# Kernel optimization log

Hardware: AMD Instinct MI355X
Metric: run time of the kernel (lower is better)

The kernel has to match this reference:

```python
import jax, jax.numpy as jnp
import numpy as np

B, T, D_IN, H, C = 16, 8192, 4, 256, 11


def setup_inputs() -> dict:
    key = jax.random.key(0)
    ks = jax.random.split(key, 9)
    sequence = jax.random.normal(ks[0], (B, T, D_IN), jnp.float32)
    # lengths in [7*T/8, T] so every sequence has mask[:,0]=True (torchcrf requirement)
    lengths = (T - jax.random.randint(ks[1], (B,), 0, T // 8)).astype(jnp.int64)
    labels = jax.random.randint(ks[2], (B, T), 0, C).astype(jnp.int64)
    W_enc = jax.random.normal(ks[3], (D_IN, H), jnp.float32) / np.float32(np.sqrt(D_IN))
    b_enc = jnp.zeros((H,), jnp.float32)
    W_emit = jax.random.normal(ks[4], (H, C), jnp.float32) / np.float32(np.sqrt(H))
    b_emit = jnp.zeros((C,), jnp.float32)
    start_trans = jax.random.normal(ks[5], (C,), jnp.float32) * 0.1
    trans = jax.random.normal(ks[6], (C, C), jnp.float32) * 0.1
    end_trans = jax.random.normal(ks[7], (C,), jnp.float32) * 0.1
    return dict(sequence=sequence, W_enc=W_enc, b_enc=b_enc, W_emit=W_emit,
                b_emit=b_emit, start_trans=start_trans, trans=trans,
                end_trans=end_trans, lengths=lengths, labels=labels)


def reference(sequence, W_enc, b_enc, W_emit, b_emit, start_trans, trans, end_trans, lengths, labels):
    # encoder (Linear + ReLU) and emission projection
    hidden = jax.nn.relu(sequence @ W_enc + b_enc)        # [B,T,H]
    em = hidden @ W_emit + b_emit                          # [B,T,C]
    mask = jnp.arange(T)[None, :] < lengths[:, None]       # [B,T] bool
    maskf = mask.astype(em.dtype)
    tags = jnp.where(labels == -100, 0, labels)            # -100 -> 0 as in compute_loss

    # ---- numerator: score of the gold path (torchcrf _compute_score) ----
    em_tag = jnp.take_along_axis(em, tags[..., None], axis=2)[..., 0]   # [B,T]
    trans_tag = trans[tags[:, :-1], tags[:, 1:]]                        # [B,T-1]
    num = start_trans[tags[:, 0]] + em_tag[:, 0]
    num = num + jnp.sum(maskf[:, 1:] * (trans_tag + em_tag[:, 1:]), axis=1)
    last_tag = tags[jnp.arange(B), lengths - 1]
    num = num + end_trans[last_tag]

    # ---- denominator: log partition via forward algorithm (torchcrf _compute_normalizer) ----
    alpha0 = start_trans[None, :] + em[:, 0]               # [B,C]
    em_rest = jnp.swapaxes(em[:, 1:], 0, 1)                # [T-1,B,C]
    mask_rest = jnp.swapaxes(mask[:, 1:], 0, 1)            # [T-1,B]

    def step(alpha, inp):
        em_t, m_t = inp
        nxt = jax.nn.logsumexp(alpha[:, :, None] + trans[None] + em_t[:, None, :], axis=1)
        return jnp.where(m_t[:, None], nxt, alpha), None

    alpha, _ = jax.lax.scan(step, alpha0, (em_rest, mask_rest))
    den = jax.nn.logsumexp(alpha + end_trans[None, :], axis=1)  # [B]

    # reduction='mean' over batch, loss = -log_likelihood
    return -jnp.mean(num - den)
```

## Files before the change

### kernel.cpp

```cpp
#include <hip/hip_runtime.h>
#include <hip/hip_bf16.h>

#define B_   16
#define T_   8192
#define H_   256
#define C_   11
#define KCH  256
#define LCH  32
#define KL   64

typedef __attribute__((ext_vector_type(8))) short short8;
typedef __attribute__((ext_vector_type(4))) float f32x4;

__global__ __launch_bounds__(256) void k_em(
    const float* __restrict__ seq, const float* __restrict__ Wenc,
    const float* __restrict__ benc, const float* __restrict__ Wemit,
    const float* __restrict__ bemit, const float* __restrict__ trans,
    const float* __restrict__ startt, const float* __restrict__ endt,
    const int* __restrict__ lengths, const int* __restrict__ labels,
    unsigned short* __restrict__ expem, float* __restrict__ numpart,
    unsigned* __restrict__ counter)
{
    __shared__ float ldsWpack[2048];
    __shared__ float ldsWemit[4096];
    __shared__ float red[4];
    int tid = threadIdx.x;
    if (blockIdx.x == 0 && tid == 0) counter[0] = 0;

    for (int idx = tid; idx < 2048; idx += 256) {
        int h = idx >> 3, s = idx & 7;
        float v = 0.f;
        if (s < 4) v = Wenc[s * H_ + h];
        else if (s == 4) v = benc[h];
        ldsWpack[idx] = v;
    }
    for (int idx = tid; idx < 4096; idx += 256) {
        int h = idx >> 4, c = idx & 15;
        ldsWemit[idx] = (c < C_) ? Wemit[h * C_ + c] : 0.f;
    }
    __syncthreads();

    int wid = tid >> 6, lane = tid & 63;
    int g = lane >> 4, li = lane & 15;
    int b0 = blockIdx.x >> 5;
    int tb0 = (blockIdx.x & 31) * 256 + wid * 64;
    size_t grow0 = (size_t)b0 * T_ + tb0;

    float4 xs[4];
#pragma unroll
    for (int tt = 0; tt < 4; tt++)
        xs[tt] = *(const float4*)(seq + (grow0 + tt * 16 + li) * 4);

    f32x4 acc[4];
#pragma unroll
    for (int tt = 0; tt < 4; tt++) acc[tt] = (f32x4){0.f, 0.f, 0.f, 0.f};

#pragma unroll 1
    for (int kb = 0; kb < 8; kb++) {
        float We[8][5], wm[8];
#pragma unroll
        for (int e = 0; e < 8; e++) {
            int h = 32 * kb + 4 * g + (e & 3) + 16 * (e >> 2);
            float4 w4 = *(const float4*)&ldsWpack[h * 8];
            We[e][0] = w4.x; We[e][1] = w4.y; We[e][2] = w4.z; We[e][3] = w4.w;
            We[e][4] = ldsWpack[h * 8 + 4];
            wm[e] = ldsWemit[h * 16 + li];
        }
        unsigned a0, a1, a2, a3;
        asm("v_cvt_pk_bf16_f32 %0, %1, %2" : "=v"(a0) : "v"(wm[0]), "v"(wm[1]));
        asm("v_cvt_pk_bf16_f32 %0, %1, %2" : "=v"(a1) : "v"(wm[2]), "v"(wm[3]));
        asm("v_cvt_pk_bf16_f32 %0, %1, %2" : "=v"(a2) : "v"(wm[4]), "v"(wm[5]));
        asm("v_cvt_pk_bf16_f32 %0, %1, %2" : "=v"(a3) : "v"(wm[6]), "v"(wm[7]));
        union { short8 s8; uint4 u4; } au;
        au.u4 = make_uint4(a0, a1, a2, a3);

#pragma unroll
        for (int tt = 0; tt < 4; tt++) {
            float4 x = xs[tt];
            float hv[8];
#pragma unroll
            for (int e = 0; e < 8; e++) {
                float h = fmaf(x.x, We[e][0],
                          fmaf(x.y, We[e][1],
                          fmaf(x.z, We[e][2],
                          fmaf(x.w, We[e][3], We[e][4]))));
                hv[e] = fmaxf(h, 0.f);
            }
            unsigned u0, u1, u2, u3;
            asm("v_cvt_pk_bf16_f32 %0, %1, %2" : "=v"(u0) : "v"(hv[0]), "v"(hv[1]));
            asm("v_cvt_pk_bf16_f32 %0, %1, %2" : "=v"(u1) : "v"(hv[2]), "v"(hv[3]));
            asm("v_cvt_pk_bf16_f32 %0, %1, %2" : "=v"(u2) : "v"(hv[4]), "v"(hv[5]));
            asm("v_cvt_pk_bf16_f32 %0, %1, %2" : "=v"(u3) : "v"(hv[6]), "v"(hv[7]));
            union { short8 s8; uint4 u4; } bfu;
            bfu.u4 = make_uint4(u0, u1, u2, u3);
            acc[tt] = __builtin_amdgcn_mfma_f32_16x16x32_bf16(au.s8, bfu.s8, acc[tt], 0, 0, 0);
        }
    }

    int len = lengths[b0];
    const int* lab = labels + (size_t)b0 * T_;
    float bm[4];
#pragma unroll
    for (int r = 0; r < 4; r++) {
        int c = 4 * g + r;
        bm[r] = (c < C_) ? bemit[c] : 0.f;
    }

    float nacc = 0.f;
#pragma unroll
    for (int tt = 0; tt < 4; tt++) {
        float em0 = acc[tt].x + bm[0];
        float em1 = acc[tt].y + bm[1];
        float em2 = acc[tt].z + bm[2];
        float em3 = acc[tt].w + bm[3];

        int t = tb0 + tt * 16 + li;
        int tg = lab[t]; tg = tg < 0 ? 0 : tg;
        if (g == (tg >> 2) && t < len) {
            int r = tg & 3;
            float emtg = r == 0 ? em0 : r == 1 ? em1 : r == 2 ? em2 : em3;
            float contrib;
            if (t == 0) {
                contrib = startt[tg] + emtg;
            } else {
                int tp = lab[t - 1]; tp = tp < 0 ? 0 : tp;
                contrib = trans[tp * C_ + tg] + emtg;
            }
            if (t == len - 1) contrib += endt[tg];
            nacc += contrib;
        }

        if (g < 3) {
            float e0 = __expf(em0), e1 = __expf(em1);
            float e2 = __expf(em2), e3 = __expf(em3);
            unsigned u0, u1;
            asm("v_cvt_pk_bf16_f32 %0, %1, %2" : "=v"(u0) : "v"(e0), "v"(e1));
            asm("v_cvt_pk_bf16_f32 %0, %1, %2" : "=v"(u1) : "v"(e2), "v"(e3));
            *(uint2*)(expem + (grow0 + tt * 16 + li) * 16 + g * 4) = make_uint2(u0, u1);
        }
    }

#pragma unroll
    for (int off = 32; off > 0; off >>= 1) nacc += __shfl_down(nacc, off);
    if (lane == 0) red[wid] = nacc;
    __syncthreads();
    if (tid == 0) numpart[blockIdx.x] = red[0] + red[1] + red[2] + red[3];
}

__device__ __forceinline__ void combineRow(const float* __restrict__ A,
                                           const float* __restrict__ Bm,
                                           float* __restrict__ D, int i)
{
    float a[C_];
#pragma unroll
    for (int kk = 0; kk < C_; kk++) a[kk] = A[i * 12 + kk];
    float als = A[i * 12 + 11];
    float m = Bm[11];
#pragma unroll
    for (int kk = 1; kk < C_; kk++) m = fmaxf(m, Bm[kk * 12 + 11]);
    float wv[C_];
#pragma unroll
    for (int kk = 0; kk < C_; kk++)
        wv[kk] = a[kk] * __expf(Bm[kk * 12 + 11] - m);
    float outv[C_];
#pragma unroll
    for (int j = 0; j < C_; j++) outv[j] = wv[0] * Bm[j];
#pragma unroll
    for (int kk = 1; kk < C_; kk++)
#pragma unroll
        for (int j = 0; j < C_; j++)
            outv[j] = fmaf(wv[kk], Bm[kk * 12 + j], outv[j]);
    float s = 0.f;
#pragma unroll
    for (int j = 0; j < C_; j++) s += outv[j];
    float rr = 1.f / s;
#pragma unroll
    for (int j = 0; j < C_; j++) D[i * 12 + j] = outv[j] * rr;
    D[i * 12 + 11] = als + m + __logf(s);
}

__global__ __launch_bounds__(256, 4) void k_chunks(
    const float* __restrict__ trans, const int* __restrict__ lengths,
    const unsigned short* __restrict__ expem, float* __restrict__ G)
{
    __shared__ float Mb[4][192];
    int tid = threadIdx.x;
    int wave = tid >> 6, lane = tid & 63;
    int i = lane & 15, g = lane >> 4;

    int bk = blockIdx.x;
    int b = bk >> 6;
    int k = ((bk & 63) << 2) | wave;
    int t0 = 1 + k * LCH;
    int len = lengths[b];
    int tl = t0 + LCH; if (len < tl) tl = len;
    int nact = tl - t0;

    const unsigned short* emp = expem + ((size_t)b * T_ + t0) * 16 + 4 * g;

    uint2 R[8][4];
#pragma unroll
    for (int q = 0; q < 16; q++)
        R[q >> 2][q & 3] = *(const uint2*)(emp + (size_t)q * 16);

    float af[4];
#pragma unroll
    for (int e = 0; e < 4; e++) {
        int kk = 4 * g + e;
        af[e] = (i < C_ && kk < C_) ? __expf(trans[kk * C_ + i]) : 0.f;
    }
    unsigned a0, a1;
    asm("v_cvt_pk_bf16_f32 %0, %1, %2" : "=v"(a0) : "v"(af[0]), "v"(af[1]));
    asm("v_cvt_pk_bf16_f32 %0, %1, %2" : "=v"(a1) : "v"(af[2]), "v"(af[3]));
    union { short8 s8; uint4 u4; } A; A.u4 = make_uint4(a0, a1, 0u, 0u);

    float p0 = (4 * g + 0 == i) ? 1.f : 0.f;
    float p1 = (4 * g + 1 == i) ? 1.f : 0.f;
    float p2 = (4 * g + 2 == i) ? 1.f : 0.f;
    float p3 = (4 * g + 3 == i) ? 1.f : 0.f;
    float ls = 0.f;

#pragma unroll
    for (int su = 0; su < 8; su++) {
        if (su < 4) {
#pragma unroll
            for (int q = 0; q < 4; q++)
                R[su + 4][q] = *(const uint2*)(emp + (size_t)((su + 4) * 4 + q) * 16);
        }
#pragma unroll
        for (int ss = 0; ss < 4; ss++) {
            if (su * 4 + ss < nact) {
                unsigned b0u, b1u;
                asm("v_cvt_pk_bf16_f32 %0, %1, %2" : "=v"(b0u) : "v"(p0), "v"(p1));
                asm("v_cvt_pk_bf16_f32 %0, %1, %2" : "=v"(b1u) : "v"(p2), "v"(p3));
                union { short8 s8; uint4 u4; } Bf; Bf.u4 = make_uint4(b0u, b1u, 0u, 0u);
                f32x4 acc = __builtin_amdgcn_mfma_f32_16x16x32_bf16(
                    A.s8, Bf.s8, (f32x4){0.f, 0.f, 0.f, 0.f}, 0, 0, 0);
                uint2 emu = R[su][ss];
                p0 = acc.x * __uint_as_float(emu.x << 16);
                p1 = acc.y * __uint_as_float(emu.x & 0xffff0000u);
                p2 = acc.z * __uint_as_float(emu.y << 16);
                p3 = acc.w * __uint_as_float(emu.y & 0xffff0000u);
            }
        }
        float part = (p0 + p1) + (p2 + p3);
        part += __shfl_xor(part, 16);
        part += __shfl_xor(part, 32);
        float r = 1.f / part;
        p0 *= r; p1 *= r; p2 *= r; p3 *= r;
        ls += __logf(part);
    }

    if (i < C_ && g < 3) {
        float w3 = (g == 2) ? ls : p3;
        *(float4*)&Mb[wave][i * 12 + 4 * g] = make_float4(p0, p1, p2, w3);
    }
    __syncthreads();

    if ((wave == 0 || wave == 2) && lane < C_)
        combineRow(Mb[wave], Mb[wave + 1], Mb[wave], lane);
    __syncthreads();

    if (wave == 0 && lane < C_) {
        float out[12];
        {
            const float* Aa = Mb[0]; const float* Bm = Mb[2];
            float a[C_];
#pragma unroll
            for (int kk = 0; kk < C_; kk++) a[kk] = Aa[lane * 12 + kk];
            float als = Aa[lane * 12 + 11];
            float m = Bm[11];
#pragma unroll
            for (int kk = 1; kk < C_; kk++) m = fmaxf(m, Bm[kk * 12 + 11]);
            float wv[C_];
#pragma unroll
            for (int kk = 0; kk < C_; kk++)
                wv[kk] = a[kk] * __expf(Bm[kk * 12 + 11] - m);
            float outv[C_];
#pragma unroll
            for (int j = 0; j < C_; j++) outv[j] = wv[0] * Bm[j];
#pragma unroll
            for (int kk = 1; kk < C_; kk++)
#pragma unroll
                for (int j = 0; j < C_; j++)
                    outv[j] = fmaf(wv[kk], Bm[kk * 12 + j], outv[j]);
            float s = 0.f;
#pragma unroll
            for (int j = 0; j < C_; j++) s += outv[j];
            float rr = 1.f / s;
#pragma unroll
            for (int j = 0; j < C_; j++) out[j] = outv[j] * rr;
            out[11] = als + m + __logf(s);
        }
        float* o = G + ((size_t)b * KL + (bk & 63)) * 132 + lane * 12;
        *(float4*)(o + 0) = make_float4(out[0], out[1], out[2], out[3]);
        *(float4*)(o + 4) = make_float4(out[4], out[5], out[6], out[7]);
        *(float4*)(o + 8) = make_float4(out[8], out[9], out[10], out[11]);
    }
}

__global__ __launch_bounds__(512, 1) void k_comb(
    const float* __restrict__ startt, const float* __restrict__ endt,
    const unsigned short* __restrict__ expem, const float* __restrict__ G0,
    const float* __restrict__ numpart, float* __restrict__ dens,
    unsigned* __restrict__ counter, float* __restrict__ out)
{
    __shared__ float M[KL * 132];
    int b = blockIdx.x, tid = threadIdx.x;

    float numb = 0.f;
    if (tid < 64) {
        float v = (tid < 32) ? numpart[b * 32 + tid] : 0.f;
#pragma unroll
        for (int off = 32; off > 0; off >>= 1) v += __shfl_down(v, off);
        numb = v;
    }

    const float4* src = (const float4*)(G0 + (size_t)b * KL * 132);
    float4* dst = (float4*)M;
#pragma unroll 4
    for (int idx = tid; idx < KL * 132 / 4; idx += 512) dst[idx] = src[idx];
    __syncthreads();

    for (int stride = 1; stride < KL; stride <<= 1) {
        int npair = KL / (2 * stride);
        for (int task = tid; task < npair * C_; task += 512) {
            int p = task / C_, i = task - p * C_;
            float* A  = M + (size_t)(2 * stride * p) * 132;
            float* Bm = M + (size_t)(2 * stride * p + stride) * 132;
            combineRow(A, Bm, A, i);
        }
        __syncthreads();
    }

    if (tid == 0) {
        const float* Cm = M;
        const unsigned short* em0 = expem + (size_t)b * T_ * 16;
        float av[C_];
        float mm = -1e30f;
#pragma unroll
        for (int i2 = 0; i2 < C_; i2++) {
            float e0 = __uint_as_float((unsigned)em0[i2] << 16);
            av[i2] = startt[i2] + __logf(e0) + Cm[i2 * 12 + 11];
            mm = fmaxf(mm, av[i2]);
        }
        float S[C_];
#pragma unroll
        for (int j = 0; j < C_; j++) S[j] = 0.f;
#pragma unroll
        for (int i2 = 0; i2 < C_; i2++) {
            float e = __expf(av[i2] - mm);
#pragma unroll
            for (int j = 0; j < C_; j++) S[j] = fmaf(e, Cm[i2 * 12 + j], S[j]);
        }
        float tot = 0.f;
#pragma unroll
        for (int j = 0; j < C_; j++) tot += S[j] * __expf(endt[j]);
        float den = __logf(tot) + mm;

        float loss = numb - den;
        __hip_atomic_store(&dens[b], loss, __ATOMIC_RELEASE, __HIP_MEMORY_SCOPE_AGENT);
        unsigned old = __hip_atomic_fetch_add(counter, 1u, __ATOMIC_ACQ_REL,
                                              __HIP_MEMORY_SCOPE_AGENT);
        if (old == B_ - 1) {
            float s = 0.f;
#pragma unroll
            for (int j = 0; j < B_; j++)
                s += __hip_atomic_load(&dens[j], __ATOMIC_ACQUIRE,
                                       __HIP_MEMORY_SCOPE_AGENT);
            out[0] = -s / (float)B_;
        }
    }
}

extern "C" void kernel_launch(void* const* d_in, const int* in_sizes, int n_in,
                              void* d_out, int out_size, void* d_ws, size_t ws_size,
                              hipStream_t stream) {
    const float* seq    = (const float*)d_in[0];
    const float* Wenc   = (const float*)d_in[1];
    const float* benc   = (const float*)d_in[2];
    const float* Wemit  = (const float*)d_in[3];
    const float* bemit  = (const float*)d_in[4];
    const float* startt = (const float*)d_in[5];
    const float* trans  = (const float*)d_in[6];
    const float* endt   = (const float*)d_in[7];
    const int*   lengths= (const int*)d_in[8];
    const int*   labels = (const int*)d_in[9];

    char* w = (char*)d_ws;
    unsigned short* expem  = (unsigned short*)w;
    float*          G0     = (float*)(w + 4194304);
    float*          numpart= (float*)(w + 4734976);
    float*          dens   = (float*)(w + 4737024);
    unsigned*       counter= (unsigned*)(w + 4737088);
    float*          out    = (float*)d_out;

    k_em<<<512, 256, 0, stream>>>(seq, Wenc, benc, Wemit, bemit, trans,
                                  startt, endt, lengths, labels,
                                  expem, numpart, counter);
    k_chunks<<<1024, 256, 0, stream>>>(trans, lengths, expem, G0);
    k_comb<<<B_, 512, 0, stream>>>(startt, endt, expem, G0, numpart,
                                   dens, counter, out);
}
```

Before: 45.23 us.

## Fuse emission and chunk-scan kernels, keeping exp-emissions in LDS

Merges the emission kernel and the chunked forward-algorithm kernel into one, so each block computes bf16 exp-emissions into shared memory and then runs the MFMA-based chunk product on 64-step chunks per wave. The global expem buffer round-trip and one kernel launch go away, and the first-timestep emissions are written to a small side buffer for the final combine. In exchange, each wave's serial chain grows from 32 to 64 steps, the fused kernel uses more LDS, and the combine tree shrinks from 64 to 32 chunks per batch.

```diff
diff --git a/kernel.cpp b/kernel.cpp
--- a/kernel.cpp
+++ b/kernel.cpp
@@ -5,25 +5,58 @@
 #define T_   8192
 #define H_   256
 #define C_   11
-#define KCH  256
-#define LCH  32
-#define KL   64
+#define KL   32
 
 typedef __attribute__((ext_vector_type(8))) short short8;
 typedef __attribute__((ext_vector_type(4))) float f32x4;
 
-__global__ __launch_bounds__(256) void k_em(
+__device__ __forceinline__ void combineRow(const float* __restrict__ A,
+                                           const float* __restrict__ Bm,
+                                           float* __restrict__ D, int i)
+{
+    float a[C_];
+#pragma unroll
+    for (int kk = 0; kk < C_; kk++) a[kk] = A[i * 12 + kk];
+    float als = A[i * 12 + 11];
+    float m = Bm[11];
+#pragma unroll
+    for (int kk = 1; kk < C_; kk++) m = fmaxf(m, Bm[kk * 12 + 11]);
+    float wv[C_];
+#pragma unroll
+    for (int kk = 0; kk < C_; kk++)
+        wv[kk] = a[kk] * __expf(Bm[kk * 12 + 11] - m);
+    float outv[C_];
+#pragma unroll
+    for (int j = 0; j < C_; j++) outv[j] = wv[0] * Bm[j];
+#pragma unroll
+    for (int kk = 1; kk < C_; kk++)
+#pragma unroll
+        for (int j = 0; j < C_; j++)
+            outv[j] = fmaf(wv[kk], Bm[kk * 12 + j], outv[j]);
+    float s = 0.f;
+#pragma unroll
+    for (int j = 0; j < C_; j++) s += outv[j];
+    float rr = 1.f / s;
+#pragma unroll
+    for (int j = 0; j < C_; j++) D[i * 12 + j] = outv[j] * rr;
+    D[i * 12 + 11] = als + m + __logf(s);
+}
+
+__global__ __launch_bounds__(256) void k_fused(
     const float* __restrict__ seq, const float* __restrict__ Wenc,
     const float* __restrict__ benc, const float* __restrict__ Wemit,
     const float* __restrict__ bemit, const float* __restrict__ trans,
     const float* __restrict__ startt, const float* __restrict__ endt,
     const int* __restrict__ lengths, const int* __restrict__ labels,
-    unsigned short* __restrict__ expem, float* __restrict__ numpart,
-    unsigned* __restrict__ counter)
+    float* __restrict__ G, float* __restrict__ numpart,
+    float* __restrict__ em0f, unsigned* __restrict__ counter)
 {
     __shared__ float ldsWpack[2048];
     __shared__ float ldsWemit[4096];
+    __shared__ unsigned emLds[256 * 8];
+    __shared__ float Mb[4][192];
     __shared__ float red[4];
+
     int tid = threadIdx.x;
     if (blockIdx.x == 0 && tid == 0) counter[0] = 0;
 
@@ -43,7 +76,9 @@
     int wid = tid >> 6, lane = tid & 63;
     int g = lane >> 4, li = lane & 15;
     int b0 = blockIdx.x >> 5;
-    int tb0 = (blockIdx.x & 31) * 256 + wid * 64;
+    int kb31 = blockIdx.x & 31;
+    int base = kb31 * 256;
+    int tb0 = base + wid * 64;
     size_t grow0 = (size_t)b0 * T_ + tb0;
 
     float4 xs[4];
@@ -130,13 +165,25 @@
             nacc += contrib;
         }
 
+        int row = wid * 64 + tt * 16 + li;
         if (g < 3) {
             float e0 = __expf(em0), e1 = __expf(em1);
             float e2 = __expf(em2), e3 = __expf(em3);
             unsigned u0, u1;
             asm("v_cvt_pk_bf16_f32 %0, %1, %2" : "=v"(u0) : "v"(e0), "v"(e1));
             asm("v_cvt_pk_bf16_f32 %0, %1, %2" : "=v"(u1) : "v"(e2), "v"(e3));
-            *(uint2*)(expem + (grow0 + tt * 16 + li) * 16 + g * 4) = make_uint2(u0, u1);
+            emLds[row * 8 + 2 * g]     = u0;
+            emLds[row * 8 + 2 * g + 1] = u1;
+            if (kb31 == 0 && row == 0) {
+                float* o0 = em0f + b0 * 12 + 4 * g;
+                o0[0] = __uint_as_float(u0 << 16);
+                o0[1] = __uint_as_float(u0 & 0xffff0000u);
+                o0[2] = __uint_as_float(u1 << 16);
+                o0[3] = __uint_as_float(u1 & 0xffff0000u);
+            }
+        } else {
+            emLds[row * 8 + 6] = 0u;
+            emLds[row * 8 + 7] = 0u;
         }
     }
 
@@ -145,102 +192,58 @@
     if (lane == 0) red[wid] = nacc;
     __syncthreads();
     if (tid == 0) numpart[blockIdx.x] = red[0] + red[1] + red[2] + red[3];
-}
-
-__device__ __forceinline__ void combineRow(const float* __restrict__ A,
-                                           const float* __restrict__ Bm,
-                                           float* __restrict__ D, int i)
-{
-    float a[C_];
-#pragma unroll
-    for (int kk = 0; kk < C_; kk++) a[kk] = A[i * 12 + kk];
-    float als = A[i * 12 + 11];
-    float m = Bm[11];
-#pragma unroll
-    for (int kk = 1; kk < C_; kk++) m = fmaxf(m, Bm[kk * 12 + 11]);
-    float wv[C_];
-#pragma unroll
-    for (int kk = 0; kk < C_; kk++)
-        wv[kk] = a[kk] * __expf(Bm[kk * 12 + 11] - m);
-    float outv[C_];
-#pragma unroll
-    for (int j = 0; j < C_; j++) outv[j] = wv[0] * Bm[j];
-#pragma unroll
-    for (int kk = 1; kk < C_; kk++)
-#pragma unroll
-        for (int j = 0; j < C_; j++)
-            outv[j] = fmaf(wv[kk], Bm[kk * 12 + j], outv[j]);
-    float s = 0.f;
-#pragma unroll
-    for (int j = 0; j < C_; j++) s += outv[j];
-    float rr = 1.f / s;
-#pragma unroll
-    for (int j = 0; j < C_; j++) D[i * 12 + j] = outv[j] * rr;
-    D[i * 12 + 11] = als + m + __logf(s);
-}
-
-__global__ __launch_bounds__(256, 4) void k_chunks(
-    const float* __restrict__ trans, const int* __restrict__ lengths,
-    const unsigned short* __restrict__ expem, float* __restrict__ G)
-{
-    __shared__ float Mb[4][192];
-    int tid = threadIdx.x;
-    int wave = tid >> 6, lane = tid & 63;
-    int i = lane & 15, g = lane >> 4;
-
-    int bk = blockIdx.x;
-    int b = bk >> 6;
-    int k = ((bk & 63) << 2) | wave;
-    int t0 = 1 + k * LCH;
-    int len = lengths[b];
-    int tl = t0 + LCH; if (len < tl) tl = len;
-    int nact = tl - t0;
-
-    const unsigned short* emp = expem + ((size_t)b * T_ + t0) * 16 + 4 * g;
-
-    uint2 R[8][4];
-#pragma unroll
-    for (int q = 0; q < 16; q++)
-        R[q >> 2][q & 3] = *(const uint2*)(emp + (size_t)q * 16);
+
+    const unsigned* erow = &emLds[wid * 64 * 8 + 2 * g];
+
+    uint2 EA[4], EB[4];
+#pragma unroll
+    for (int q = 0; q < 4; q++) EA[q] = *(const uint2*)(erow + q * 8);
 
     float af[4];
 #pragma unroll
     for (int e = 0; e < 4; e++) {
         int kk = 4 * g + e;
-        af[e] = (i < C_ && kk < C_) ? __expf(trans[kk * C_ + i]) : 0.f;
-    }
-    unsigned a0, a1;
-    asm("v_cvt_pk_bf16_f32 %0, %1, %2" : "=v"(a0) : "v"(af[0]), "v"(af[1]));
-    asm("v_cvt_pk_bf16_f32 %0, %1, %2" : "=v"(a1) : "v"(af[2]), "v"(af[3]));
-    union { short8 s8; uint4 u4; } A; A.u4 = make_uint4(a0, a1, 0u, 0u);
-
-    float p0 = (4 * g + 0 == i) ? 1.f : 0.f;
-    float p1 = (4 * g + 1 == i) ? 1.f : 0.f;
-    float p2 = (4 * g + 2 == i) ? 1.f : 0.f;
-    float p3 = (4 * g + 3 == i) ? 1.f : 0.f;
+        af[e] = (li < C_ && kk < C_) ? __expf(trans[kk * C_ + li]) : 0.f;
+    }
+    unsigned fa0, fa1;
+    asm("v_cvt_pk_bf16_f32 %0, %1, %2" : "=v"(fa0) : "v"(af[0]), "v"(af[1]));
+    asm("v_cvt_pk_bf16_f32 %0, %1, %2" : "=v"(fa1) : "v"(af[2]), "v"(af[3]));
+    union { short8 s8; uint4 u4; } A; A.u4 = make_uint4(fa0, fa1, 0u, 0u);
+
+    float p0 = (4 * g + 0 == li) ? 1.f : 0.f;
+    float p1 = (4 * g + 1 == li) ? 1.f : 0.f;
+    float p2 = (4 * g + 2 == li) ? 1.f : 0.f;
+    float p3 = (4 * g + 3 == li) ? 1.f : 0.f;
     float ls = 0.f;
 
 #pragma unroll
-    for (int su = 0; su < 8; su++) {
-        if (su < 4) {
-#pragma unroll
-            for (int q = 0; q < 4; q++)
-                R[su + 4][q] = *(const uint2*)(emp + (size_t)((su + 4) * 4 + q) * 16);
+    for (int grp = 0; grp < 16; grp++) {
+        if (grp < 15) {
+            if ((grp & 1) == 0) {
+#pragma unroll
+                for (int q = 0; q < 4; q++)
+                    EB[q] = *(const uint2*)(erow + ((grp + 1) * 4 + q) * 8);
+            } else {
+#pragma unroll
+                for (int q = 0; q < 4; q++)
+                    EA[q] = *(const uint2*)(erow + ((grp + 1) * 4 + q) * 8);
+            }
         }
 #pragma unroll
         for (int ss = 0; ss < 4; ss++) {
-            if (su * 4 + ss < nact) {
+            int t = base + wid * 64 + grp * 4 + ss;
+            if (t >= 1 && t < len) {
                 unsigned b0u, b1u;
                 asm("v_cvt_pk_bf16_f32 %0, %1, %2" : "=v"(b0u) : "v"(p0), "v"(p1));
                 asm("v_cvt_pk_bf16_f32 %0, %1, %2" : "=v"(b1u) : "v"(p2), "v"(p3));
                 union { short8 s8; uint4 u4; } Bf; Bf.u4 = make_uint4(b0u, b1u, 0u, 0u);
-                f32x4 acc = __builtin_amdgcn_mfma_f32_16x16x32_bf16(
+                f32x4 pa = __builtin_amdgcn_mfma_f32_16x16x32_bf16(
                     A.s8, Bf.s8, (f32x4){0.f, 0.f, 0.f, 0.f}, 0, 0, 0);
-                uint2 emu = R[su][ss];
-                p0 = acc.x * __uint_as_float(emu.x << 16);
-                p1 = acc.y * __uint_as_float(emu.x & 0xffff0000u);
-                p2 = acc.z * __uint_as_float(emu.y << 16);
-                p3 = acc.w * __uint_as_float(emu.y & 0xffff0000u);
+                uint2 emu = ((grp & 1) == 0) ? EA[ss] : EB[ss];
+                p0 = pa.x * __uint_as_float(emu.x << 16);
+                p1 = pa.y * __uint_as_float(emu.x & 0xffff0000u);
+                p2 = pa.z * __uint_as_float(emu.y << 16);
+                p3 = pa.w * __uint_as_float(emu.y & 0xffff0000u);
             }
         }
         float part = (p0 + p1) + (p2 + p3);
@@ -251,17 +254,17 @@
         ls += __logf(part);
     }
 
-    if (i < C_ && g < 3) {
+    if (li < C_ && g < 3) {
         float w3 = (g == 2) ? ls : p3;
-        *(float4*)&Mb[wave][i * 12 + 4 * g] = make_float4(p0, p1, p2, w3);
+        *(float4*)&Mb[wid][li * 12 + 4 * g] = make_float4(p0, p1, p2, w3);
     }
     __syncthreads();
 
-    if ((wave == 0 || wave == 2) && lane < C_)
-        combineRow(Mb[wave], Mb[wave + 1], Mb[wave], lane);
+    if ((wid == 0 || wid == 2) && lane < C_)
+        combineRow(Mb[wid], Mb[wid + 1], Mb[wid], lane);
     __syncthreads();
 
-    if (wave == 0 && lane < C_) {
+    if (wid == 0 && lane < C_) {
         float out[12];
         {
             const float* Aa = Mb[0]; const float* Bm = Mb[2];
@@ -292,7 +295,7 @@
             for (int j = 0; j < C_; j++) out[j] = outv[j] * rr;
             out[11] = als + m + __logf(s);
         }
-        float* o = G + ((size_t)b * KL + (bk & 63)) * 132 + lane * 12;
+        float* o = G + ((size_t)b0 * KL + kb31) * 132 + lane * 12;
         *(float4*)(o + 0) = make_float4(out[0], out[1], out[2], out[3]);
         *(float4*)(o + 4) = make_float4(out[4], out[5], out[6], out[7]);
         *(float4*)(o + 8) = make_float4(out[8], out[9], out[10], out[11]);
@@ -301,7 +304,7 @@
 
 __global__ __launch_bounds__(512, 1) void k_comb(
     const float* __restrict__ startt, const float* __restrict__ endt,
-    const unsigned short* __restrict__ expem, const float* __restrict__ G0,
+    const float* __restrict__ em0f, const float* __restrict__ G0,
     const float* __restrict__ numpart, float* __restrict__ dens,
     unsigned* __restrict__ counter, float* __restrict__ out)
 {
@@ -318,7 +321,7 @@
 
     const float4* src = (const float4*)(G0 + (size_t)b * KL * 132);
     float4* dst = (float4*)M;
-#pragma unroll 4
+#pragma unroll 2
     for (int idx = tid; idx < KL * 132 / 4; idx += 512) dst[idx] = src[idx];
     __syncthreads();
 
@@ -335,13 +338,12 @@
 
     if (tid == 0) {
         const float* Cm = M;
-        const unsigned short* em0 = expem + (size_t)b * T_ * 16;
+        const float* e0 = em0f + b * 12;
         float av[C_];
         float mm = -1e30f;
 #pragma unroll
         for (int i2 = 0; i2 < C_; i2++) {
-            float e0 = __uint_as_float((unsigned)em0[i2] << 16);
-            av[i2] = startt[i2] + __logf(e0) + Cm[i2 * 12 + 11];
+            av[i2] = startt[i2] + __logf(e0[i2]) + Cm[i2 * 12 + 11];
             mm = fmaxf(mm, av[i2]);
         }
         float S[C_];
@@ -388,17 +390,16 @@
     const int*   labels = (const int*)d_in[9];
 
     char* w = (char*)d_ws;
-    unsigned short* expem  = (unsigned short*)w;
-    float*          G0     = (float*)(w + 4194304);
-    float*          numpart= (float*)(w + 4734976);
-    float*          dens   = (float*)(w + 4737024);
-    unsigned*       counter= (unsigned*)(w + 4737088);
-    float*          out    = (float*)d_out;
-
-    k_em<<<512, 256, 0, stream>>>(seq, Wenc, benc, Wemit, bemit, trans,
-                                  startt, endt, lengths, labels,
-                                  expem, numpart, counter);
-    k_chunks<<<1024, 256, 0, stream>>>(trans, lengths, expem, G0);
-    k_comb<<<B_, 512, 0, stream>>>(startt, endt, expem, G0, numpart,
+    float*    G       = (float*)w;
+    float*    numpart = (float*)(w + 270336);
+    float*    dens    = (float*)(w + 272384);
+    float*    em0f    = (float*)(w + 272448);
+    unsigned* counter = (unsigned*)(w + 273216);
+    float*    out     = (float*)d_out;
+
+    k_fused<<<512, 256, 0, stream>>>(seq, Wenc, benc, Wemit, bemit, trans,
+                                     startt, endt, lengths, labels,
+                                     G, numpart, em0f, counter);
+    k_comb<<<B_, 512, 0, stream>>>(startt, endt, em0f, G, numpart,
                                    dens, counter, out);
 }
```

Measured after the change: 39.16 us, median of 3. -13.4%, faster.
